# Performance work log

Hardware: AMD Instinct MI355X
Metric: run time of the kernel (lower is better)

The kernel has to match this reference:

```python
import jax, jax.numpy as jnp
import numpy as np

D_MODEL = 1024
NUM_HEADS = 16
D_K = D_MODEL // NUM_HEADS


def setup_inputs() -> dict:
    key = jax.random.key(0)
    ks = jax.random.split(key, 11)
    B, S = 2, 2048
    scale = 1.0 / np.sqrt(D_MODEL)
    inp = {
        "Q": jax.random.normal(ks[0], (B, S, D_MODEL), jnp.float32),
        "K": jax.random.normal(ks[1], (B, S, D_MODEL), jnp.float32),
        "V": jax.random.normal(ks[2], (B, S, D_MODEL), jnp.float32),
        "W_q": jax.random.normal(ks[3], (D_MODEL, D_MODEL), jnp.float32) * scale,
        "b_q": jnp.zeros((D_MODEL,), jnp.float32),
        "W_k": jax.random.normal(ks[4], (D_MODEL, D_MODEL), jnp.float32) * scale,
        "b_k": jnp.zeros((D_MODEL,), jnp.float32),
        "W_v": jax.random.normal(ks[5], (D_MODEL, D_MODEL), jnp.float32) * scale,
        "b_v": jnp.zeros((D_MODEL,), jnp.float32),
        "W_o": jax.random.normal(ks[6], (D_MODEL, D_MODEL), jnp.float32) * scale,
        "b_o": jnp.zeros((D_MODEL,), jnp.float32),
    }
    return inp


def _split_heads(x):
    # [B, S, D] -> [B, H, S, d_k]
    B, S, _ = x.shape
    return x.reshape(B, S, NUM_HEADS, D_K).transpose(0, 2, 1, 3)


def reference(Q, K, V, W_q, b_q, W_k, b_k, W_v, b_v, W_o, b_o):
    # linear projections (torch Linear: x @ W.T + b)
    q = _split_heads(Q @ W_q.T + b_q)
    k = _split_heads(K @ W_k.T + b_k)
    v = _split_heads(V @ W_v.T + b_v)
    # scaled dot-product attention, full [B,H,S,S] scores as in source
    scores = jnp.einsum("bhqd,bhkd->bhqk", q, k) / jnp.sqrt(jnp.float32(D_K))
    probs = jax.nn.softmax(scores, axis=-1)
    ctx = jnp.einsum("bhqk,bhkd->bhqd", probs, v)
    # combine heads: [B,H,S,d_k] -> [B,S,D]
    B, H, S, d = ctx.shape
    ctx = ctx.transpose(0, 2, 1, 3).reshape(B, S, H * d)
    return ctx @ W_o.T + b_o
```

## Files before the change

kernel.cpp:

```cpp
#include <hip/hip_runtime.h>
#include <hip/hip_bf16.h>

typedef unsigned short u16;
typedef unsigned int u32;
typedef short s16x8 __attribute__((ext_vector_type(8)));
typedef float f32x4 __attribute__((ext_vector_type(4)));
typedef float f32x16 __attribute__((ext_vector_type(16)));
typedef u32 u32x4 __attribute__((ext_vector_type(4)));

#define DEV static __device__ __forceinline__

DEV u16 bf16_rne(float f) {
  u32 u = __builtin_bit_cast(u32, f);
  u += 0x7fffu + ((u >> 16) & 1u);
  return (u16)(u >> 16);
}

#define GLDS16(g, l)                                                           \
  __builtin_amdgcn_global_load_lds(                                           \
      (const __attribute__((address_space(1))) void*)(g),                     \
      (__attribute__((address_space(3))) void*)(l), 16, 0, 0)

__global__ void cvt7_kernel(const float* a0, const float* a1, const float* a2,
                            const float* w0, const float* w1, const float* w2,
                            const float* w3, u16* da0, u16* da1, u16* da2,
                            u16* dw0, u16* dw1, u16* dw2, u16* dw3, int n4a,
                            int n4w) {
  const int z = blockIdx.y;
  const float* s;
  u16* d;
  int n4;
  if (z < 3) {
    s = (z == 0) ? a0 : (z == 1) ? a1 : a2;
    d = (z == 0) ? da0 : (z == 1) ? da1 : da2;
    n4 = n4a;
  } else {
    const int zz = z - 3;
    s = (zz == 0) ? w0 : (zz == 1) ? w1 : (zz == 2) ? w2 : w3;
    d = (zz == 0) ? dw0 : (zz == 1) ? dw1 : (zz == 2) ? dw2 : dw3;
    n4 = n4w;
  }
  int i = blockIdx.x * blockDim.x + threadIdx.x;
  if (i < n4) {
    float4 v = reinterpret_cast<const float4*>(s)[i];
    ushort4 o;
    o.x = bf16_rne(v.x);
    o.y = bf16_rne(v.y);
    o.z = bf16_rne(v.z);
    o.w = bf16_rne(v.w);
    reinterpret_cast<ushort4*>(d)[i] = o;
  }
}

__global__ __launch_bounds__(256, 3) void gemm_qkv(
    const u16* __restrict__ A0, const u16* __restrict__ A1,
    const u16* __restrict__ A2, const u16* __restrict__ W0,
    const u16* __restrict__ W1, const u16* __restrict__ W2,
    const float* __restrict__ bias0, const float* __restrict__ bias1,
    const float* __restrict__ bias2, u16* __restrict__ C0,
    u16* __restrict__ C1v, u16* __restrict__ C2, int M, int N, int K) {
  const int z = blockIdx.z;
  const u16* A = (z == 0) ? A0 : (z == 1) ? A1 : A2;
  const u16* W = (z == 0) ? W0 : (z == 1) ? W1 : W2;
  const float* bias = (z == 0) ? bias0 : (z == 1) ? bias1 : bias2;
  u16* Cout = (z == 0) ? C0 : (z == 1) ? C1v : C2;
  const float escale = (z == 0) ? 0.125f * 1.44269504088896f : 1.0f;

  __shared__ __align__(16) u16 As[128 * 64];
  __shared__ __align__(16) u16 Ws[128 * 64];
  const int tid = threadIdx.x;
  const int lane = tid & 63;
  const int w = tid >> 6;
  const int wr = w >> 1, wc = w & 1;
  const int l15 = lane & 15, l4 = lane >> 4;
  const int m0 = blockIdx.x * 128, n0 = blockIdx.y * 128;

  f32x4 acc[4][4] = {};
  float bv[4];
#pragma unroll
  for (int fc = 0; fc < 4; ++fc) bv[fc] = bias[n0 + wc * 64 + fc * 16 + l15];

  for (int kt = 0; kt < K; kt += 64) {
    __syncthreads();
#pragma unroll
    for (int i = 0; i < 4; ++i) {
      const int ch = i * 256 + tid;
      const int row = ch >> 3, cl = ch & 7;
      GLDS16(A + (size_t)(m0 + row) * K + kt + ((cl ^ (row & 7)) * 8),
             As + (size_t)(i * 256 + w * 64) * 8);
    }
#pragma unroll
    for (int i = 0; i < 4; ++i) {
      const int ch = i * 256 + tid;
      const int row = ch >> 3, cl = ch & 7;
      GLDS16(W + (size_t)(n0 + row) * K + kt + ((cl ^ (row & 7)) * 8),
             Ws + (size_t)(i * 256 + w * 64) * 8);
    }
    __syncthreads();
#pragma unroll
    for (int ks = 0; ks < 2; ++ks) {
      const int sw = (ks * 4 + l4) ^ (l15 & 7);
      s16x8 a[4], b[4];
#pragma unroll
      for (int f = 0; f < 4; ++f)
        a[f] = *(const s16x8*)(As + (size_t)((wr * 64 + f * 16 + l15) * 8 + sw) * 8);
#pragma unroll
      for (int f = 0; f < 4; ++f)
        b[f] = *(const s16x8*)(Ws + (size_t)((wc * 64 + f * 16 + l15) * 8 + sw) * 8);
#pragma unroll
      for (int fr = 0; fr < 4; ++fr)
#pragma unroll
        for (int fc = 0; fc < 4; ++fc)
          acc[fr][fc] = __builtin_amdgcn_mfma_f32_16x16x32_bf16(
              a[fr], b[fc], acc[fr][fc], 0, 0, 0);
    }
  }

  if (z == 2) {
#pragma unroll
    for (int fr = 0; fr < 4; ++fr) {
      const int m = m0 + wr * 64 + fr * 16 + l4 * 4;
      const int bb = m >> 11, s = m & 2047;
#pragma unroll
      for (int fc = 0; fc < 4; ++fc) {
        const int n = n0 + wc * 64 + fc * 16 + l15;
        const int hh = n >> 6, dd = n & 63;
        ushort4 o;
        o.x = bf16_rne(acc[fr][fc][0] + bv[fc]);
        o.y = bf16_rne(acc[fr][fc][1] + bv[fc]);
        o.z = bf16_rne(acc[fr][fc][2] + bv[fc]);
        o.w = bf16_rne(acc[fr][fc][3] + bv[fc]);
        *(ushort4*)(Cout + (((size_t)(bb * 16 + hh) * 64 + dd) * 2048 + s)) = o;
      }
    }
  } else {
#pragma unroll
    for (int fr = 0; fr < 4; ++fr) {
      const int mrow = m0 + wr * 64 + fr * 16 + l4 * 4;
#pragma unroll
      for (int fc = 0; fc < 4; ++fc) {
        const int ncol = n0 + wc * 64 + fc * 16 + l15;
#pragma unroll
        for (int r = 0; r < 4; ++r)
          Cout[(size_t)(mrow + r) * N + ncol] =
              bf16_rne((acc[fr][fc][r] + bv[fc]) * escale);
      }
    }
  }
}

__global__ __launch_bounds__(256, 4) void gemm_o(
    const u16* __restrict__ A, const u16* __restrict__ W,
    const float* __restrict__ bias, float* __restrict__ Cout, int M, int N,
    int K) {
  __shared__ __align__(16) u16 As[128 * 64];
  __shared__ __align__(16) u16 Ws[64 * 64];
  const int tid = threadIdx.x;
  const int lane = tid & 63;
  const int w = tid >> 6;
  const int wr = w >> 1, wc = w & 1;
  const int l15 = lane & 15, l4 = lane >> 4;
  const int m0 = blockIdx.x * 128, n0 = blockIdx.y * 64;

  f32x4 acc[4][2] = {};
  float bv[2];
#pragma unroll
  for (int fc = 0; fc < 2; ++fc) bv[fc] = bias[n0 + wc * 32 + fc * 16 + l15];

  for (int kt = 0; kt < K; kt += 64) {
    __syncthreads();
#pragma unroll
    for (int i = 0; i < 4; ++i) {
      const int ch = i * 256 + tid;
      const int row = ch >> 3, cl = ch & 7;
      GLDS16(A + (size_t)(m0 + row) * K + kt + ((cl ^ (row & 7)) * 8),
             As + (size_t)(i * 256 + w * 64) * 8);
    }
#pragma unroll
    for (int i = 0; i < 2; ++i) {
      const int ch = i * 256 + tid;
      const int row = ch >> 3, cl = ch & 7;
      GLDS16(W + (size_t)(n0 + row) * K + kt + ((cl ^ (row & 7)) * 8),
             Ws + (size_t)(i * 256 + w * 64) * 8);
    }
    __syncthreads();
#pragma unroll
    for (int ks = 0; ks < 2; ++ks) {
      const int sw = (ks * 4 + l4) ^ (l15 & 7);
      s16x8 a[4], b[2];
#pragma unroll
      for (int f = 0; f < 4; ++f)
        a[f] = *(const s16x8*)(As + (size_t)((wr * 64 + f * 16 + l15) * 8 + sw) * 8);
#pragma unroll
      for (int f = 0; f < 2; ++f)
        b[f] = *(const s16x8*)(Ws + (size_t)((wc * 32 + f * 16 + l15) * 8 + sw) * 8);
#pragma unroll
      for (int fr = 0; fr < 4; ++fr)
#pragma unroll
        for (int fc = 0; fc < 2; ++fc)
          acc[fr][fc] = __builtin_amdgcn_mfma_f32_16x16x32_bf16(
              a[fr], b[fc], acc[fr][fc], 0, 0, 0);
    }
  }

#pragma unroll
  for (int fr = 0; fr < 4; ++fr) {
    const int mrow = m0 + wr * 64 + fr * 16 + l4 * 4;
#pragma unroll
    for (int fc = 0; fc < 2; ++fc) {
      const int ncol = n0 + wc * 32 + fc * 16 + l15;
#pragma unroll
      for (int r = 0; r < 4; ++r)
        Cout[(size_t)(mrow + r) * N + ncol] = acc[fr][fc][r] + bv[fc];
    }
  }
}

__global__ __launch_bounds__(512, 4) void attn_fused(
    const u16* __restrict__ qp, const u16* __restrict__ kp,
    const u16* __restrict__ vt, u16* __restrict__ ctx) {
  const int S = 2048, D = 1024;
  const int bh = blockIdx.x;
  const int qt = blockIdx.y;
  const int tid = threadIdx.x, lane = tid & 63, w = tid >> 6;
  const int l31 = lane & 31, l5 = lane >> 5;
  const int g = tid >> 8;
  const int tl = tid & 255;
  const int wl = tl >> 6;
  const int wq = w & 3;

  __shared__ __align__(16) u16 SM[32768];

  const size_t qkbase = ((size_t)(bh >> 4) * S) * D + (size_t)(bh & 15) * 64;
  const size_t vbase = (size_t)bh * 64 * S;

  const int q = qt * 128 + wq * 32 + l31;
  s16x8 qf[4];
#pragma unroll
  for (int ks = 0; ks < 4; ++ks)
    qf[ks] = *(const s16x8*)(qp + qkbase + (size_t)q * D + ks * 16 + l5 * 8);

  u32x4 onesw;
  onesw[0] = onesw[1] = onesw[2] = onesw[3] = 0x3F803F80u;
  const s16x8 ones = __builtin_bit_cast(s16x8, onesw);

  f32x16 octx[2] = {};
  f32x16 lacc = {};

  auto stage = [&](int buf, int ti) {
    const int kv0 = (g * 16 + ti) * 64;
    u16* Kd = SM + g * 16384 + buf * 4096;
    u16* Vd = SM + g * 16384 + 8192 + buf * 4096;
#pragma unroll
    for (int i = 0; i < 2; ++i) {
      const int gch = i * 256 + tl;
      const int kv = gch >> 3, cc = gch & 7;
      GLDS16(kp + qkbase + (size_t)(kv0 + kv) * D + ((cc ^ (kv & 7)) << 3),
             Kd + (size_t)(i * 256 + wl * 64) * 8);
    }
#pragma unroll
    for (int i = 0; i < 2; ++i) {
      const int gch = i * 256 + tl;
      const int d = gch >> 3, cc = gch & 7;
      GLDS16(vt + vbase + (size_t)d * S + kv0 + ((cc ^ (d & 7)) << 3),
             Vd + (size_t)(i * 256 + wl * 64) * 8);
    }
  };

  stage(0, 0);
  const int NT = 16;
  for (int t = 0; t < NT; ++t) {
    __syncthreads();
    if (t + 1 < NT) stage((t + 1) & 1, t + 1);
    const u16* Kb = SM + g * 16384 + (t & 1) * 4096;
    const u16* Vb = SM + g * 16384 + 8192 + (t & 1) * 4096;

    f32x16 sc[2] = {};
#pragma unroll
    for (int ks = 0; ks < 4; ++ks) {
      __builtin_amdgcn_s_setprio(1);
#pragma unroll
      for (int fk = 0; fk < 2; ++fk) {
        const int kv = fk * 32 + l31;
        const int c = (ks << 1) + l5;
        const s16x8 kf =
            *(const s16x8*)(Kb + (size_t)(kv * 8 + (c ^ (kv & 7))) * 8);
        sc[fk] = __builtin_amdgcn_mfma_f32_32x32x16_bf16(kf, qf[ks], sc[fk],
                                                         0, 0, 0);
      }
      __builtin_amdgcn_s_setprio(0);
    }

#pragma unroll
    for (int c4 = 0; c4 < 4; ++c4) {
      const int fk = c4 >> 1, hf = c4 & 1;
      float p[8];
#pragma unroll
      for (int j = 0; j < 8; ++j)
        p[j] = __builtin_amdgcn_exp2f(sc[fk][hf * 8 + j]);
      u32 x0, x1, y0, y1;
      asm("v_cvt_pk_bf16_f32 %0, %1, %2" : "=v"(x0) : "v"(p[0]), "v"(p[1]));
      asm("v_cvt_pk_bf16_f32 %0, %1, %2" : "=v"(x1) : "v"(p[2]), "v"(p[3]));
      asm("v_cvt_pk_bf16_f32 %0, %1, %2" : "=v"(y0) : "v"(p[4]), "v"(p[5]));
      asm("v_cvt_pk_bf16_f32 %0, %1, %2" : "=v"(y1) : "v"(p[6]), "v"(p[7]));
      asm("v_permlane32_swap_b32 %0, %1" : "+v"(x0), "+v"(y0));
      asm("v_permlane32_swap_b32 %0, %1" : "+v"(x1), "+v"(y1));
      u32x4 bw;
      bw[0] = x0; bw[1] = x1; bw[2] = y0; bw[3] = y1;
      const s16x8 pb = __builtin_bit_cast(s16x8, bw);
      __builtin_amdgcn_s_setprio(1);
      lacc = __builtin_amdgcn_mfma_f32_32x32x16_bf16(ones, pb, lacc, 0, 0, 0);
#pragma unroll
      for (int fd = 0; fd < 2; ++fd) {
        const int d = fd * 32 + l31;
        const int c = (c4 << 1) + l5;
        const s16x8 vf =
            *(const s16x8*)(Vb + (size_t)(d * 8 + (c ^ (d & 7))) * 8);
        octx[fd] = __builtin_amdgcn_mfma_f32_32x32x16_bf16(vf, pb, octx[fd],
                                                           0, 0, 0);
      }
      __builtin_amdgcn_s_setprio(0);
    }
  }

  const float lpart = lacc[0];

  __syncthreads();
  float* scr = (float*)(void*)SM;
  if (g == 1) {
    float* dst = scr + ((size_t)wq * 64 + lane) * 33;
#pragma unroll
    for (int fd = 0; fd < 2; ++fd)
#pragma unroll
      for (int r = 0; r < 16; ++r) dst[fd * 16 + r] = octx[fd][r];
    dst[32] = lpart;
  }
  __syncthreads();
  if (g == 0) {
    const float* src = scr + ((size_t)wq * 64 + lane) * 33;
    const float linv = 1.f / (lpart + src[32]);
#pragma unroll
    for (int fd = 0; fd < 2; ++fd)
#pragma unroll
      for (int gg = 0; gg < 4; ++gg) {
        ushort4 o;
        o.x = bf16_rne((octx[fd][gg * 4 + 0] + src[fd * 16 + gg * 4 + 0]) * linv);
        o.y = bf16_rne((octx[fd][gg * 4 + 1] + src[fd * 16 + gg * 4 + 1]) * linv);
        o.z = bf16_rne((octx[fd][gg * 4 + 2] + src[fd * 16 + gg * 4 + 2]) * linv);
        o.w = bf16_rne((octx[fd][gg * 4 + 3] + src[fd * 16 + gg * 4 + 3]) * linv);
        *(ushort4*)(ctx + qkbase + (size_t)q * D + fd * 32 + gg * 8 + l5 * 4) =
            o;
      }
  }
}

extern "C" void kernel_launch(void* const* d_in, const int* in_sizes, int n_in,
                              void* d_out, int out_size, void* d_ws,
                              size_t ws_size, hipStream_t stream) {
  (void)in_sizes; (void)n_in; (void)out_size; (void)ws_size;
  const float* Q = (const float*)d_in[0];
  const float* K = (const float*)d_in[1];
  const float* V = (const float*)d_in[2];
  const float* Wq = (const float*)d_in[3];
  const float* bq = (const float*)d_in[4];
  const float* Wk = (const float*)d_in[5];
  const float* bk = (const float*)d_in[6];
  const float* Wv = (const float*)d_in[7];
  const float* bv = (const float*)d_in[8];
  const float* Wo = (const float*)d_in[9];
  const float* bo = (const float*)d_in[10];

  const int B = 2, S = 2048, D = 1024, H = 16;
  const int M = B * S;
  const size_t NE = (size_t)M * D;
  const size_t WE = (size_t)D * D;

  u16* Qb = (u16*)d_ws;
  u16* Kb = Qb + NE;
  u16* Vb = Kb + NE;
  u16* qp = Vb + NE;
  u16* kp = qp + NE;
  u16* vtb = kp + NE;
  u16* Wqb = vtb + NE;
  u16* Wkb = Wqb + WE;
  u16* Wvb = Wkb + WE;
  u16* Wob = Wvb + WE;

  const int n4 = (int)(NE / 4), nb = (n4 + 255) / 256;
  const int w4 = (int)(WE / 4);
  cvt7_kernel<<<dim3(nb, 7), 256, 0, stream>>>(Q, K, V, Wq, Wk, Wv, Wo, Qb, Kb,
                                               Vb, Wqb, Wkb, Wvb, Wob, n4, w4);

  dim3 gg(M / 128, D / 128, 3);
  gemm_qkv<<<gg, 256, 0, stream>>>(Qb, Kb, Vb, Wqb, Wkb, Wvb, bq, bk, bv, qp,
                                   kp, vtb, M, D, D);

  dim3 ga(B * H, S / 128);
  attn_fused<<<ga, 512, 0, stream>>>(qp, kp, vtb, Qb);

  dim3 go(M / 128, D / 64);
  gemm_o<<<go, 256, 0, stream>>>(Qb, Wob, bo, (float*)d_out, M, D, D);
}
```

Measured before the change: 106.2 us.

## Double-buffer LDS tiles in QKV and output projection GEMMs

Both projection GEMMs now keep two LDS buffers for the A and W tiles. The next K-tile is issued with global_load_lds right after the barrier and lands while MFMAs run on the current tile, leaving one barrier per iteration instead of two. This is meant to hide global-to-LDS load latency behind the matrix math. It doubles LDS use per block, so launch bounds drop from 3 to 2 (QKV) and from 4 to 3 (output) blocks per CU, which lowers occupancy.

```diff
diff --git a/kernel.cpp b/kernel.cpp
--- a/kernel.cpp
+++ b/kernel.cpp
@@ -52,7 +52,7 @@
   }
 }
 
-__global__ __launch_bounds__(256, 3) void gemm_qkv(
+__global__ __launch_bounds__(256, 2) void gemm_qkv(
     const u16* __restrict__ A0, const u16* __restrict__ A1,
     const u16* __restrict__ A2, const u16* __restrict__ W0,
     const u16* __restrict__ W1, const u16* __restrict__ W2,
@@ -66,8 +66,8 @@
   u16* Cout = (z == 0) ? C0 : (z == 1) ? C1v : C2;
   const float escale = (z == 0) ? 0.125f * 1.44269504088896f : 1.0f;
 
-  __shared__ __align__(16) u16 As[128 * 64];
-  __shared__ __align__(16) u16 Ws[128 * 64];
+  __shared__ __align__(16) u16 As[2][128 * 64];
+  __shared__ __align__(16) u16 Ws[2][128 * 64];
   const int tid = threadIdx.x;
   const int lane = tid & 63;
   const int w = tid >> 6;
@@ -80,33 +80,40 @@
 #pragma unroll
   for (int fc = 0; fc < 4; ++fc) bv[fc] = bias[n0 + wc * 64 + fc * 16 + l15];
 
-  for (int kt = 0; kt < K; kt += 64) {
-    __syncthreads();
+  auto stage = [&](int buf, int kt) {
 #pragma unroll
     for (int i = 0; i < 4; ++i) {
       const int ch = i * 256 + tid;
       const int row = ch >> 3, cl = ch & 7;
       GLDS16(A + (size_t)(m0 + row) * K + kt + ((cl ^ (row & 7)) * 8),
-             As + (size_t)(i * 256 + w * 64) * 8);
+             &As[buf][(size_t)(i * 256 + w * 64) * 8]);
     }
 #pragma unroll
     for (int i = 0; i < 4; ++i) {
       const int ch = i * 256 + tid;
       const int row = ch >> 3, cl = ch & 7;
       GLDS16(W + (size_t)(n0 + row) * K + kt + ((cl ^ (row & 7)) * 8),
-             Ws + (size_t)(i * 256 + w * 64) * 8);
-    }
+             &Ws[buf][(size_t)(i * 256 + w * 64) * 8]);
+    }
+  };
+
+  const int NT = K >> 6;
+  stage(0, 0);
+  for (int t = 0; t < NT; ++t) {
     __syncthreads();
+    if (t + 1 < NT) stage((t + 1) & 1, (t + 1) * 64);
+    const u16* Ab = As[t & 1];
+    const u16* Wb = Ws[t & 1];
 #pragma unroll
     for (int ks = 0; ks < 2; ++ks) {
       const int sw = (ks * 4 + l4) ^ (l15 & 7);
       s16x8 a[4], b[4];
 #pragma unroll
       for (int f = 0; f < 4; ++f)
-        a[f] = *(const s16x8*)(As + (size_t)((wr * 64 + f * 16 + l15) * 8 + sw) * 8);
+        a[f] = *(const s16x8*)(Ab + (size_t)((wr * 64 + f * 16 + l15) * 8 + sw) * 8);
 #pragma unroll
       for (int f = 0; f < 4; ++f)
-        b[f] = *(const s16x8*)(Ws + (size_t)((wc * 64 + f * 16 + l15) * 8 + sw) * 8);
+        b[f] = *(const s16x8*)(Wb + (size_t)((wc * 64 + f * 16 + l15) * 8 + sw) * 8);
 #pragma unroll
       for (int fr = 0; fr < 4; ++fr)
 #pragma unroll
@@ -149,12 +156,12 @@
   }
 }
 
-__global__ __launch_bounds__(256, 4) void gemm_o(
+__global__ __launch_bounds__(256, 3) void gemm_o(
     const u16* __restrict__ A, const u16* __restrict__ W,
     const float* __restrict__ bias, float* __restrict__ Cout, int M, int N,
     int K) {
-  __shared__ __align__(16) u16 As[128 * 64];
-  __shared__ __align__(16) u16 Ws[64 * 64];
+  __shared__ __align__(16) u16 As[2][128 * 64];
+  __shared__ __align__(16) u16 Ws[2][64 * 64];
   const int tid = threadIdx.x;
   const int lane = tid & 63;
   const int w = tid >> 6;
@@ -167,33 +174,40 @@
 #pragma unroll
   for (int fc = 0; fc < 2; ++fc) bv[fc] = bias[n0 + wc * 32 + fc * 16 + l15];
 
-  for (int kt = 0; kt < K; kt += 64) {
-    __syncthreads();
+  auto stage = [&](int buf, int kt) {
 #pragma unroll
     for (int i = 0; i < 4; ++i) {
       const int ch = i * 256 + tid;
       const int row = ch >> 3, cl = ch & 7;
       GLDS16(A + (size_t)(m0 + row) * K + kt + ((cl ^ (row & 7)) * 8),
-             As + (size_t)(i * 256 + w * 64) * 8);
+             &As[buf][(size_t)(i * 256 + w * 64) * 8]);
     }
 #pragma unroll
     for (int i = 0; i < 2; ++i) {
       const int ch = i * 256 + tid;
       const int row = ch >> 3, cl = ch & 7;
       GLDS16(W + (size_t)(n0 + row) * K + kt + ((cl ^ (row & 7)) * 8),
-             Ws + (size_t)(i * 256 + w * 64) * 8);
-    }
+             &Ws[buf][(size_t)(i * 256 + w * 64) * 8]);
+    }
+  };
+
+  const int NT = K >> 6;
+  stage(0, 0);
+  for (int t = 0; t < NT; ++t) {
     __syncthreads();
+    if (t + 1 < NT) stage((t + 1) & 1, (t + 1) * 64);
+    const u16* Ab = As[t & 1];
+    const u16* Wb = Ws[t & 1];
 #pragma unroll
     for (int ks = 0; ks < 2; ++ks) {
       const int sw = (ks * 4 + l4) ^ (l15 & 7);
       s16x8 a[4], b[2];
 #pragma unroll
       for (int f = 0; f < 4; ++f)
-        a[f] = *(const s16x8*)(As + (size_t)((wr * 64 + f * 16 + l15) * 8 + sw) * 8);
+        a[f] = *(const s16x8*)(Ab + (size_t)((wr * 64 + f * 16 + l15) * 8 + sw) * 8);
 #pragma unroll
       for (int f = 0; f < 2; ++f)
-        b[f] = *(const s16x8*)(Ws + (size_t)((wc * 32 + f * 16 + l15) * 8 + sw) * 8);
+        b[f] = *(const s16x8*)(Wb + (size_t)((wc * 32 + f * 16 + l15) * 8 + sw) * 8);
 #pragma unroll
       for (int fr = 0; fr < 4; ++fr)
 #pragma unroll
```

Result: slower. 115.1 us (+8.4%).
